# Optimization experiments

Hardware: AMD Instinct MI355X
Metric: run time of the kernel (lower is better)

The kernel has to match this reference:

```python
import jax, jax.numpy as jnp
import numpy as np

DIM = 1024
NUM_HEADS = 16
HEAD_DIM = DIM // NUM_HEADS
SCALE = HEAD_DIM ** -0.5


def setup_inputs() -> dict:
    key = jax.random.key(0)
    k_x, k_wqkv, k_bqkv, k_wp, k_bp = jax.random.split(key, 5)
    B, C, D = 4, 1024, DIM
    x = jax.random.normal(k_x, (B, C, D), dtype=jnp.float32)
    # nn.Linear stores weight as (out, in); we keep (in, out) for x @ W
    w_qkv = jax.random.normal(k_wqkv, (D, 3 * D), dtype=jnp.float32) * (D ** -0.5)
    b_qkv = jax.random.normal(k_bqkv, (3 * D,), dtype=jnp.float32) * 0.02
    w_proj = jax.random.normal(k_wp, (D, D), dtype=jnp.float32) * (D ** -0.5)
    b_proj = jax.random.normal(k_bp, (D,), dtype=jnp.float32) * 0.02
    return {"x": x, "w_qkv": w_qkv, "b_qkv": b_qkv, "w_proj": w_proj, "b_proj": b_proj}


def reference(x, w_qkv, b_qkv, w_proj, b_proj):
    B, C, D = x.shape
    H, Hd = NUM_HEADS, HEAD_DIM
    qkv = x @ w_qkv + b_qkv                       # (B, C, 3D)
    qkv = qkv.reshape(B, C, 3, H, Hd)
    q = qkv[:, :, 0].transpose(0, 2, 1, 3)        # (B, H, C, Hd)
    k = qkv[:, :, 1].transpose(0, 2, 1, 3)
    v = qkv[:, :, 2].transpose(0, 2, 1, 3)
    attn = jnp.einsum('bhqd,bhkd->bhqk', q, k) * SCALE
    attn = jax.nn.softmax(attn, axis=-1)
    out = jnp.einsum('bhqk,bhkd->bhqd', attn, v)  # (B, H, C, Hd)
    out = out.transpose(0, 2, 1, 3).reshape(B, C, D)
    return out @ w_proj + b_proj
```

## Files before the change

### kernel.cpp

```cpp
#include <hip/hip_runtime.h>
#include <cstdint>

#define BB 4
#define CC 1024
#define DD 1024
#define HH 16
#define HD 64
#define NH3 3072

typedef __attribute__((ext_vector_type(8))) short short8;
typedef __attribute__((ext_vector_type(4))) float f32x4;
typedef __attribute__((ext_vector_type(16))) float f32x16;

#define MFMA16(a, b, c) __builtin_amdgcn_mfma_f32_16x16x32_bf16(a, b, c, 0, 0, 0)
#define MFMA32(a, b, c) __builtin_amdgcn_mfma_f32_32x32x16_bf16(a, b, c, 0, 0, 0)
#define EXP2 __builtin_amdgcn_exp2f

__device__ __forceinline__ void glds16(const void* g, void* l) {
    __builtin_amdgcn_global_load_lds(
        (const __attribute__((address_space(1))) void*)g,
        (__attribute__((address_space(3))) void*)l, 16, 0, 0);
}

__device__ __forceinline__ ushort f2bf(float f) {
    union { float f; uint32_t u; } v; v.f = f;
    uint32_t r = v.u + 0x7FFF + ((v.u >> 16) & 1);
    return (ushort)(r >> 16);
}

__device__ __forceinline__ uint32_t pack2bf(float a, float b) {
    uint32_t ua = __float_as_uint(a), ub = __float_as_uint(b);
    ua += 0x7FFF + ((ua >> 16) & 1);
    ub += 0x7FFF + ((ub >> 16) & 1);
    return __builtin_amdgcn_perm(ua, ub, 0x03020706);
}

__global__ __launch_bounds__(256)
void prep_kernel(const float* __restrict__ x, ushort* __restrict__ xbf,
                 const float* __restrict__ wqkv, ushort* __restrict__ wqkvT,
                 const float* __restrict__ wprj, ushort* __restrict__ wprjT)
{
    __shared__ float Ts[64 * 65];
    const int blk = blockIdx.x;
    const int t = threadIdx.x;

    if (blk < 4096) {
        int i = blk * 256 + t;
        float4 v = ((const float4*)x)[i];
        ushort4 o;
        o.x = f2bf(v.x); o.y = f2bf(v.y); o.z = f2bf(v.z); o.w = f2bf(v.w);
        ((ushort4*)xbf)[i] = o;
        return;
    }

    const float* in; ushort* outp; int K, N, n0, k0;
    if (blk < 4864) {
        int bx = blk - 4096;
        in = wqkv; outp = wqkvT; K = DD; N = NH3;
        n0 = (bx % 48) * 64; k0 = (bx / 48) * 64;
    } else {
        int bx = blk - 4864;
        in = wprj; outp = wprjT; K = DD; N = DD;
        n0 = (bx % 16) * 64; k0 = (bx / 16) * 64;
    }
    #pragma unroll
    for (int i = 0; i < 16; ++i) {
        int idx = t + i * 256;
        int r = idx >> 6, c = idx & 63;
        Ts[r * 65 + c] = in[(size_t)(k0 + r) * N + n0 + c];
    }
    __syncthreads();
    #pragma unroll
    for (int i = 0; i < 16; ++i) {
        int idx = t + i * 256;
        int rr = idx >> 6, cc = idx & 63;
        outp[(size_t)(n0 + rr) * K + k0 + cc] = f2bf(Ts[cc * 65 + rr]);
    }
}

template<int MODE, int MT, int SWZ>
__global__ __launch_bounds__(256)
void gemm_bt(const ushort* __restrict__ A, const ushort* __restrict__ Bt,
             const float* __restrict__ bias, float* __restrict__ Cf,
             ushort* __restrict__ qb, ushort* __restrict__ kb, ushort* __restrict__ vtb,
             int M, int N, int K)
{
    constexpr int MI = MT / 32;
    __shared__ ushort As[3][MT * 32];
    __shared__ ushort Bs[3][128 * 32];

    const int tid = threadIdx.x;
    const int wid = tid >> 6, lane = tid & 63;
    const int quad = lane >> 4, l15 = lane & 15;

    int bxi, byi;
    if (SWZ) {
        const int flat = blockIdx.x;
        const int cpx = gridDim.x >> 3;
        const int f2 = (flat & 7) * cpx + (flat >> 3);
        const int nbx = N / 128;
        bxi = f2 % nbx; byi = f2 / nbx;
    } else {
        bxi = blockIdx.x; byi = blockIdx.y;
    }
    const int m0 = byi * MT, n0 = bxi * 128;
    const int wm = (wid >> 1) * (MT / 2), wn = (wid & 1) * 64;

    const int sr = lane >> 2;
    const int sc = lane & 3;

    const int ar0 = wid * (MT / 4) + sr;
    const int acg0 = sc ^ ((ar0 >> 1) & 3);
    const int acg1 = sc ^ (((ar0 + 16) >> 1) & 3);
    const ushort* Ar0 = A + (size_t)(m0 + ar0) * K + acg0 * 8;
    const ushort* Ar1 = A + (size_t)(m0 + ar0 + 16) * K + acg1 * 8;
    const int br0 = wid * 32 + sr;
    const int bcg0 = sc ^ ((br0 >> 1) & 3);
    const int bcg1 = sc ^ (((br0 + 16) >> 1) & 3);
    const ushort* Br0 = Bt + (size_t)(n0 + br0) * K + bcg0 * 8;
    const ushort* Br1 = Bt + (size_t)(n0 + br0 + 16) * K + bcg1 * 8;

    f32x4 acc[MI][4];
    #pragma unroll
    for (int i = 0; i < MI; ++i)
        #pragma unroll
        for (int j = 0; j < 4; ++j) acc[i][j] = (f32x4)(0.0f);

#define GSTAGE(kn, bidx) do { \
        glds16(Ar0 + (kn), &As[bidx][(wid * (MT / 4)) * 32]); \
        glds16(Br0 + (kn), &Bs[bidx][(wid * 32) * 32]); \
        if (MT == 128) glds16(Ar1 + (kn), &As[bidx][(wid * 32 + 16) * 32]); \
        glds16(Br1 + (kn), &Bs[bidx][(wid * 32 + 16) * 32]); } while (0)

    GSTAGE(0, 0);
    GSTAGE(32, 1);

    int cur = 0;
    for (int k0 = 0; k0 < K; k0 += 32) {
        if (k0 + 32 < K) {
            if (MT == 128)
                asm volatile("s_waitcnt vmcnt(4)\n\ts_barrier" ::: "memory");
            else
                asm volatile("s_waitcnt vmcnt(3)\n\ts_barrier" ::: "memory");
        } else {
            asm volatile("s_waitcnt vmcnt(0)\n\ts_barrier" ::: "memory");
        }
        if (k0 + 64 < K) {
            const int nb = (cur >= 1) ? cur - 1 : 2;
            GSTAGE(k0 + 64, nb);
        }

        short8 af[MI], bf[4];
        #pragma unroll
        for (int i = 0; i < MI; ++i) {
            int row = wm + i * 16 + l15;
            af[i] = *(const short8*)(&As[cur][row * 32 + (quad ^ ((row >> 1) & 3)) * 8]);
        }
        #pragma unroll
        for (int j = 0; j < 4; ++j) {
            int col = wn + j * 16 + l15;
            bf[j] = *(const short8*)(&Bs[cur][col * 32 + (quad ^ ((col >> 1) & 3)) * 8]);
        }
        #pragma unroll
        for (int i = 0; i < MI; ++i)
            #pragma unroll
            for (int j = 0; j < 4; ++j)
                acc[i][j] = MFMA16(af[i], bf[j], acc[i][j]);

        cur = (cur == 2) ? 0 : cur + 1;
    }
#undef GSTAGE

    if (MODE == 0) {
        #pragma unroll
        for (int i = 0; i < MI; ++i) {
            int row = m0 + wm + i * 16 + quad * 4;
            #pragma unroll
            for (int j = 0; j < 4; ++j) {
                int col = n0 + wn + j * 16 + l15;
                float bv = bias[col];
                #pragma unroll
                for (int r = 0; r < 4; ++r)
                    Cf[(size_t)(row + r) * N + col] = acc[i][j][r] + bv;
            }
        }
    } else {
        #pragma unroll
        for (int j = 0; j < 4; ++j) {
            int n = n0 + wn + j * 16 + l15;
            int three = n >> 10;
            int h = (n >> 6) & 15;
            int hd = n & 63;
            float scale = (three == 0) ? 0.1803368801f : 1.0f;
            float bv = bias[n];
            #pragma unroll
            for (int i = 0; i < MI; ++i) {
                int row = m0 + wm + i * 16 + quad * 4;
                #pragma unroll
                for (int r = 0; r < 4; ++r) {
                    int m = row + r;
                    int b = m >> 10, c = m & 1023;
                    ushort val = f2bf((acc[i][j][r] + bv) * scale);
                    if (three == 0)
                        qb[((size_t)((b * HH + h) * CC) + c) * HD + hd] = val;
                    else if (three == 1)
                        kb[((size_t)((b * HH + h) * CC) + c) * HD + hd] = val;
                    else
                        vtb[((size_t)((b * HH + h) * HD) + hd) * CC + c] = val;
                }
            }
        }
    }
}

__global__ __launch_bounds__(256)
void attn_mfma9(const ushort* __restrict__ qb, const ushort* __restrict__ kbuf,
                const ushort* __restrict__ vt, ushort* __restrict__ attnb)
{
    __shared__ ushort lds[3 * 4096 + 4 * 4096];
    const uint K0 = 0, K1 = 4096, K2 = 8192;
    const uint V0 = 12288, V1 = 16384, V2 = 20480, V3 = 24576;

    const int tid = threadIdx.x;
    const int wid = tid >> 6, lane = tid & 63;
    const int l31 = lane & 31, hi = lane >> 5;
    const int bh = blockIdx.x & 63;
    const int qt = blockIdx.x >> 6;
    const int q0 = qt * 128;
    const int b = bh >> 4, h = bh & 15;

    const ushort* Qp  = qb  + ((size_t)bh * CC + q0) * HD;
    const ushort* Kp  = kbuf + (size_t)bh * CC * HD;
    const ushort* Vtp = vt  + (size_t)bh * HD * CC;

    short8 qf[4];
    {
        const int qrow = wid * 32 + l31;
        #pragma unroll
        for (int s = 0; s < 4; ++s)
            qf[s] = *(const short8*)(Qp + (size_t)qrow * HD + s * 16 + hi * 8);
    }

    const int sr = lane >> 3;
    const int sc = lane & 7;
    const int kr = wid * 16 + sr;
    const int cgA = sc ^ (kr & 7);
    const int cgB = sc ^ ((kr + 8) & 7);
    const ushort* Kr0 = Kp  + (size_t)kr * HD + cgA * 8;
    const ushort* Kr1 = Kp  + (size_t)(kr + 8) * HD + cgB * 8;
    const ushort* Vr0 = Vtp + (size_t)kr * CC + cgA * 8;
    const ushort* Vr1 = Vtp + (size_t)(kr + 8) * CC + cgB * 8;

    const uint stg0 = (wid * 16) * 64;
    const uint stg1 = (wid * 16 + 8) * 64;

    glds16(Kr0, lds + K0 + stg0);
    glds16(Kr1, lds + K0 + stg1);
    glds16(Vr0, lds + V0 + stg0);
    glds16(Vr1, lds + V0 + stg1);
    glds16(Kr0 + (size_t)64 * HD, lds + K1 + stg0);
    glds16(Kr1 + (size_t)64 * HD, lds + K1 + stg1);
    glds16(Vr0 + 64, lds + V1 + stg0);
    glds16(Vr1 + 64, lds + V1 + stg1);

    f32x16 oacc[2];
    oacc[0] = (f32x16)(0.0f);
    oacc[1] = (f32x16)(0.0f);
    float lsum = 0.0f;

    uint ksC = K0, ksN = K1, ksF = K2;
    uint vsP = V3, vsC = V0, vsN = V1, vsF = V2;

    uint32_t pkA[2][8], pkB[2][8];

#define APV9(PKP) do { \
        __builtin_amdgcn_s_setprio(1); \
        _Pragma("unroll") \
        for (int m = 0; m < 4; ++m) { \
            const int kb2_ = m >> 1, s4_ = (m & 1) * 4; \
            uint32_t x0_ = PKP[kb2_][s4_ + 0], x1_ = PKP[kb2_][s4_ + 1]; \
            uint32_t y0_ = PKP[kb2_][s4_ + 2], y1_ = PKP[kb2_][s4_ + 3]; \
            asm("v_permlane32_swap_b32 %0, %1" : "+v"(x0_), "+v"(y0_)); \
            asm("v_permlane32_swap_b32 %0, %1" : "+v"(x1_), "+v"(y1_)); \
            union { short8 s; uint32_t u[4]; } pu_; \
            pu_.u[0] = x0_; pu_.u[1] = x1_; pu_.u[2] = y0_; pu_.u[3] = y1_; \
            _Pragma("unroll") \
            for (int db_ = 0; db_ < 2; ++db_) { \
                int hr_ = db_ * 32 + l31; \
                short8 vf_ = *(const short8*)(lds + vsP + hr_ * 64 + \
                                (((m * 2 + hi) ^ (hr_ & 7)) * 8)); \
                oacc[db_] = MFMA32(pu_.s, vf_, oacc[db_]); \
            } \
        } \
        __builtin_amdgcn_s_setprio(0); \
    } while (0)

#define AITER9(kt, PKP, PKC) do { \
        if ((kt) < 15) asm volatile("s_waitcnt vmcnt(4)\n\ts_barrier" ::: "memory"); \
        else           asm volatile("s_waitcnt vmcnt(0)\n\ts_barrier" ::: "memory"); \
        if ((kt) < 14) {                      \
            const int koff_ = ((kt) + 2) * 64; \
            glds16(Kr0 + (size_t)koff_ * HD, lds + ksF + stg0); \
            glds16(Kr1 + (size_t)koff_ * HD, lds + ksF + stg1); \
            glds16(Vr0 + koff_,              lds + vsF + stg0); \
            glds16(Vr1 + koff_,              lds + vsF + stg1); \
        } \
        if ((kt) > 0) { APV9(PKP); } \
         \
        _Pragma("unroll") \
        for (int kb2 = 0; kb2 < 2; ++kb2) { \
            f32x16 sacc = (f32x16)(0.0f); \
            _Pragma("unroll") \
            for (int s = 0; s < 4; ++s) { \
                int row = kb2 * 32 + l31; \
                short8 kf = *(const short8*)(lds + ksC + row * 64 + \
                                (((s * 2 + hi) ^ (row & 7)) * 8)); \
                sacc = MFMA32(kf, qf[s], sacc); \
            } \
            float p_[16]; \
            _Pragma("unroll") \
            for (int r = 0; r < 16; ++r) p_[r] = EXP2(sacc[r]); \
            lsum += ((((p_[0] + p_[1]) + (p_[2] + p_[3])) + \
                      ((p_[4] + p_[5]) + (p_[6] + p_[7]))) + \
                     (((p_[8] + p_[9]) + (p_[10] + p_[11])) + \
                      ((p_[12] + p_[13]) + (p_[14] + p_[15])))); \
            _Pragma("unroll") \
            for (int g = 0; g < 4; ++g) { \
                PKC[kb2][2 * g]     = pack2bf(p_[4 * g],     p_[4 * g + 1]); \
                PKC[kb2][2 * g + 1] = pack2bf(p_[4 * g + 2], p_[4 * g + 3]); \
            } \
        } \
         \
        uint t_ = ksC; ksC = ksN; ksN = ksF; ksF = t_; \
        t_ = vsP; vsP = vsC; vsC = vsN; vsN = vsF; vsF = t_; \
    } while (0)

    for (int k2 = 0; k2 < 8; ++k2) {
        AITER9(2 * k2,     pkA, pkB);
        AITER9(2 * k2 + 1, pkB, pkA);
    }

    APV9(pkA);
#undef AITER9
#undef APV9

    lsum += __shfl_xor(lsum, 32);

    #pragma unroll
    for (int r = 0; r < 16; ++r) {
        int qm = (r & 3) + 8 * (r >> 2) + 4 * hi;
        float inv = 1.0f / __shfl(lsum, qm);
        int c = q0 + wid * 32 + qm;
        #pragma unroll
        for (int dblk = 0; dblk < 2; ++dblk) {
            int d = h * 64 + dblk * 32 + l31;
            attnb[((size_t)(b * CC + c)) * DD + d] = f2bf(oacc[dblk][r] * inv);
        }
    }
}

extern "C" void kernel_launch(void* const* d_in, const int* in_sizes, int n_in,
                              void* d_out, int out_size, void* d_ws, size_t ws_size,
                              hipStream_t stream)
{
    (void)in_sizes; (void)n_in; (void)out_size; (void)ws_size;
    const float* x      = (const float*)d_in[0];
    const float* w_qkv  = (const float*)d_in[1];
    const float* b_qkv  = (const float*)d_in[2];
    const float* w_proj = (const float*)d_in[3];
    const float* b_proj = (const float*)d_in[4];
    float* out = (float*)d_out;

    ushort* p = (ushort*)d_ws;
    ushort* xbf   = p;  p += (size_t)4 * 1024 * 1024;
    ushort* wqkvT = p;  p += (size_t)3 * 1024 * 1024;
    ushort* wprjT = p;  p += (size_t)1 * 1024 * 1024;
    ushort* qbuf  = p;  p += (size_t)4 * 1024 * 1024;
    ushort* kbuf  = p;  p += (size_t)4 * 1024 * 1024;
    ushort* vtb   = p;  p += (size_t)4 * 1024 * 1024;
    ushort* attnb = p;  p += (size_t)4 * 1024 * 1024;

    prep_kernel<<<5120, 256, 0, stream>>>(x, xbf, w_qkv, wqkvT, w_proj, wprjT);

    gemm_bt<1, 128, 0><<<dim3(NH3 / 128, (BB * CC) / 128), 256, 0, stream>>>(
        xbf, wqkvT, b_qkv, nullptr, qbuf, kbuf, vtb, BB * CC, NH3, DD);

    attn_mfma9<<<512, 256, 0, stream>>>(qbuf, kbuf, vtb, attnb);

    gemm_bt<0, 64, 1><<<512, 256, 0, stream>>>(
        attnb, wprjT, b_proj, out, nullptr, nullptr, nullptr, BB * CC, DD, DD);
}
```

Measured before the change: 172.0 us.

## Replace QKV GEMM with 256x256-tile 8-wave ping-pong pipelined kernel

Adds a new QKV projection GEMM that uses 256x256 output tiles with 512 threads (8 waves) and splits each K-step into four phases. Each phase interleaves LDS fragment reads, async global-to-LDS staging of the next tile quarters, and prioritized MFMA bursts, with double-buffered LDS. The goal is higher data reuse per tile and better overlap of memory and compute than the previous 128x128 generic GEMM. In exchange it uses 128KB of LDS and many accumulator registers, and the grid shrinks to 192 blocks, which may underfill the GPU's CUs.

```diff
diff --git a/kernel.cpp b/kernel.cpp
--- a/kernel.cpp
+++ b/kernel.cpp
@@ -15,6 +15,7 @@
 #define MFMA16(a, b, c) __builtin_amdgcn_mfma_f32_16x16x32_bf16(a, b, c, 0, 0, 0)
 #define MFMA32(a, b, c) __builtin_amdgcn_mfma_f32_32x32x16_bf16(a, b, c, 0, 0, 0)
 #define EXP2 __builtin_amdgcn_exp2f
+#define SB0 __builtin_amdgcn_sched_barrier(0)
 
 __device__ __forceinline__ void glds16(const void* g, void* l) {
     __builtin_amdgcn_global_load_lds(
@@ -213,6 +214,157 @@
     }
 }
 
+__global__ __launch_bounds__(512)
+void gemm_qkv8p(const ushort* __restrict__ A, const ushort* __restrict__ Bt,
+                const float* __restrict__ bias,
+                ushort* __restrict__ qb, ushort* __restrict__ kb,
+                ushort* __restrict__ vtb)
+{
+    constexpr int K = DD;
+    constexpr int NKT = K / 64;
+    __shared__ ushort lds[2][32768];
+
+    const int tid = threadIdx.x;
+    const int wid = tid >> 6, lane = tid & 63;
+    const int quad = lane >> 4, l15 = lane & 15;
+    const int m0 = blockIdx.y * 256, n0 = blockIdx.x * 256;
+    const int wm = (wid >> 2) * 128, wn = (wid & 3) * 64;
+
+    const int srow = wid * 8 + (lane >> 3);
+    const int scol = ((lane & 7) ^ (lane >> 3)) * 8;
+    const ushort* gA0a = A + (size_t)(m0 + srow) * K + scol;
+    const ushort* gA0b = A + (size_t)(m0 + 64 + srow) * K + scol;
+    const ushort* gA1a = A + (size_t)(m0 + 128 + srow) * K + scol;
+    const ushort* gA1b = A + (size_t)(m0 + 192 + srow) * K + scol;
+    const ushort* gB0a = Bt + (size_t)(n0 + srow) * K + scol;
+    const ushort* gB0b = Bt + (size_t)(n0 + 64 + srow) * K + scol;
+    const ushort* gB1a = Bt + (size_t)(n0 + 128 + srow) * K + scol;
+    const ushort* gB1b = Bt + (size_t)(n0 + 192 + srow) * K + scol;
+    const int wof = wid * 512;
+
+#define STG_A0(kt, b) do { glds16(gA0a + (kt) * 64, &lds[b][0     + wof]); \
+                           glds16(gA0b + (kt) * 64, &lds[b][4096  + wof]); } while (0)
+#define STG_A1(kt, b) do { glds16(gA1a + (kt) * 64, &lds[b][8192  + wof]); \
+                           glds16(gA1b + (kt) * 64, &lds[b][12288 + wof]); } while (0)
+#define STG_B0(kt, b) do { glds16(gB0a + (kt) * 64, &lds[b][16384 + wof]); \
+                           glds16(gB0b + (kt) * 64, &lds[b][20480 + wof]); } while (0)
+#define STG_B1(kt, b) do { glds16(gB1a + (kt) * 64, &lds[b][24576 + wof]); \
+                           glds16(gB1b + (kt) * 64, &lds[b][28672 + wof]); } while (0)
+
+    f32x4 acc[8][4];
+    #pragma unroll
+    for (int i = 0; i < 8; ++i)
+        #pragma unroll
+        for (int j = 0; j < 4; ++j) acc[i][j] = (f32x4)(0.0f);
+
+    STG_A0(0, 0); STG_A1(0, 0); STG_B0(0, 0); STG_B1(0, 0);
+    STG_B0(1, 1); STG_B1(1, 1);
+    asm volatile("s_waitcnt vmcnt(4)" ::: "memory");
+    __builtin_amdgcn_s_barrier();
+
+#define RD_A(dst, base_i, buf_) \
+    _Pragma("unroll") \
+    for (int i = 0; i < 4; ++i) { \
+        const int R = wm + (base_i + i) * 16 + l15; \
+        _Pragma("unroll") \
+        for (int s = 0; s < 2; ++s) \
+            dst[i][s] = *(const short8*)(&lds[buf_][R * 64 + (((s * 4 + quad) ^ (R & 7)) * 8)]); \
+    }
+#define RD_B(dst, base_j, buf_) \
+    _Pragma("unroll") \
+    for (int j = 0; j < 2; ++j) { \
+        const int C = wn + (base_j + j) * 16 + l15; \
+        _Pragma("unroll") \
+        for (int s = 0; s < 2; ++s) \
+            dst[j][s] = *(const short8*)(&lds[buf_][16384 + C * 64 + (((s * 4 + quad) ^ (C & 7)) * 8)]); \
+    }
+#define MM(AF, BF, MH, NH) \
+    _Pragma("unroll") \
+    for (int i = 0; i < 4; ++i) \
+        _Pragma("unroll") \
+        for (int j = 0; j < 2; ++j) \
+            _Pragma("unroll") \
+            for (int s = 0; s < 2; ++s) \
+                acc[(MH) * 4 + i][(NH) * 2 + j] = MFMA16(AF[i][s], BF[j][s], acc[(MH) * 4 + i][(NH) * 2 + j]);
+
+#define PHASE_TAIL() do { \
+        SB0; __builtin_amdgcn_s_barrier(); \
+        asm volatile("s_waitcnt lgkmcnt(0)" ::: "memory"); SB0; } while (0)
+
+    for (int kt = 0; kt < NKT; ++kt) {
+        const int buf = kt & 1;
+        short8 a0[4][2], a1[4][2], b0[2][2], b1[2][2];
+
+        RD_A(a0, 0, buf);
+        RD_B(b0, 0, buf);
+        if (kt + 1 < NKT) STG_A0(kt + 1, buf ^ 1);
+        PHASE_TAIL();
+        __builtin_amdgcn_s_setprio(1);
+        MM(a0, b0, 0, 0);
+        __builtin_amdgcn_s_setprio(0); SB0;
+        __builtin_amdgcn_s_barrier();
+
+        RD_B(b1, 2, buf);
+        if (kt + 1 < NKT) STG_A1(kt + 1, buf ^ 1);
+        PHASE_TAIL();
+        __builtin_amdgcn_s_setprio(1);
+        MM(a0, b1, 0, 1);
+        __builtin_amdgcn_s_setprio(0); SB0;
+        __builtin_amdgcn_s_barrier();
+
+        RD_A(a1, 4, buf);
+        if (kt + 2 < NKT) STG_B0(kt + 2, buf);
+        PHASE_TAIL();
+        __builtin_amdgcn_s_setprio(1);
+        MM(a1, b0, 1, 0);
+        __builtin_amdgcn_s_setprio(0); SB0;
+        __builtin_amdgcn_s_barrier();
+
+        if (kt + 2 < NKT) STG_B1(kt + 2, buf);
+        SB0; __builtin_amdgcn_s_barrier();
+        __builtin_amdgcn_s_setprio(1);
+        MM(a1, b1, 1, 1);
+        __builtin_amdgcn_s_setprio(0); SB0;
+        if (kt <= 13)      asm volatile("s_waitcnt vmcnt(4)" ::: "memory");
+        else if (kt == 14) asm volatile("s_waitcnt vmcnt(0)" ::: "memory");
+        __builtin_amdgcn_s_barrier();
+    }
+#undef PHASE_TAIL
+#undef MM
+#undef RD_A
+#undef RD_B
+#undef STG_A0
+#undef STG_A1
+#undef STG_B0
+#undef STG_B1
+
+    #pragma unroll
+    for (int j = 0; j < 4; ++j) {
+        int n = n0 + wn + j * 16 + l15;
+        int three = n >> 10;
+        int h = (n >> 6) & 15;
+        int hd = n & 63;
+        float scale = (three == 0) ? 0.1803368801f : 1.0f;
+        float bv = bias[n];
+        #pragma unroll
+        for (int i = 0; i < 8; ++i) {
+            int row = m0 + wm + i * 16 + quad * 4;
+            #pragma unroll
+            for (int r = 0; r < 4; ++r) {
+                int m = row + r;
+                int b = m >> 10, c = m & 1023;
+                ushort val = f2bf((acc[i][j][r] + bv) * scale);
+                if (three == 0)
+                    qb[((size_t)((b * HH + h) * CC) + c) * HD + hd] = val;
+                else if (three == 1)
+                    kb[((size_t)((b * HH + h) * CC) + c) * HD + hd] = val;
+                else
+                    vtb[((size_t)((b * HH + h) * HD) + hd) * CC + c] = val;
+            }
+        }
+    }
+}
+
 __global__ __launch_bounds__(256)
 void attn_mfma9(const ushort* __restrict__ qb, const ushort* __restrict__ kbuf,
                 const ushort* __restrict__ vt, ushort* __restrict__ attnb)
@@ -306,7 +458,6 @@
             glds16(Vr1 + koff_,              lds + vsF + stg1); \
         } \
         if ((kt) > 0) { APV9(PKP); } \
-         \
         _Pragma("unroll") \
         for (int kb2 = 0; kb2 < 2; ++kb2) { \
             f32x16 sacc = (f32x16)(0.0f); \
@@ -330,7 +481,6 @@
                 PKC[kb2][2 * g + 1] = pack2bf(p_[4 * g + 2], p_[4 * g + 3]); \
             } \
         } \
-         \
         uint t_ = ksC; ksC = ksN; ksN = ksF; ksF = t_; \
         t_ = vsP; vsP = vsC; vsC = vsN; vsN = vsF; vsF = t_; \
     } while (0)
@@ -382,8 +532,8 @@
 
     prep_kernel<<<5120, 256, 0, stream>>>(x, xbf, w_qkv, wqkvT, w_proj, wprjT);
 
-    gemm_bt<1, 128, 0><<<dim3(NH3 / 128, (BB * CC) / 128), 256, 0, stream>>>(
-        xbf, wqkvT, b_qkv, nullptr, qbuf, kbuf, vtb, BB * CC, NH3, DD);
+    gemm_qkv8p<<<dim3(NH3 / 256, (BB * CC) / 256), 512, 0, stream>>>(
+        xbf, wqkvT, b_qkv, qbuf, kbuf, vtb);
 
     attn_mfma9<<<512, 256, 0, stream>>>(qbuf, kbuf, vtb, attnb);
 
```

Measured after the change: 188.2 us. +9.4%, slower.
